# Kernel tuning notes

Hardware: AMD Instinct MI355X
Metric: run time of the kernel (lower is better)

The kernel has to match this reference:

```python
import jax, jax.numpy as jnp
import numpy as np

B, NW = 1024, 300
N = NW // 3          # 100 tokens (keypoints)
E = 5                # token dim after cat of PE(2): 3 + 2
H, D, L = 4, 64, 3   # heads, d_attention, layers


def setup_inputs() -> dict:
    key = jax.random.key(0)
    ks = jax.random.split(key, 8)
    s = jnp.float32(0.1)
    x = jax.random.normal(ks[0], (B, NW), dtype=jnp.float32)
    Wq = jax.random.normal(ks[1], (L, H, D, E), dtype=jnp.float32) * s  # per-head W_Q (no bias)
    Wk = jax.random.normal(ks[2], (L, H, D, E), dtype=jnp.float32) * s
    Wv = jax.random.normal(ks[3], (L, H, D, E), dtype=jnp.float32) * s
    Wo = jax.random.normal(ks[4], (L, E, H * D), dtype=jnp.float32) * s  # MHA output proj (no bias)
    Wf = jax.random.normal(ks[5], (L, E, E), dtype=jnp.float32) * s      # FFN linear
    bf = jax.random.normal(ks[6], (L, E), dtype=jnp.float32) * s
    g1 = jnp.ones((L, E), dtype=jnp.float32)
    b1 = jnp.zeros((L, E), dtype=jnp.float32)
    g2 = jnp.ones((L, E), dtype=jnp.float32)
    b2 = jnp.zeros((L, E), dtype=jnp.float32)
    return dict(x=x, Wq=Wq, Wk=Wk, Wv=Wv, Wo=Wo, Wf=Wf, bf=bf,
                g1=g1, b1=b1, g2=g2, b2=b2)


def _layer_norm(x, g, b, eps=1e-5):
    mu = jnp.mean(x, axis=-1, keepdims=True)
    var = jnp.mean((x - mu) ** 2, axis=-1, keepdims=True)  # biased, like torch LN
    return (x - mu) / jnp.sqrt(var + eps) * g + b


def reference(x, Wq, Wk, Wv, Wo, Wf, bf, g1, b1, g2, b2):
    kp = x.reshape(B, N, 3)                      # 'b (n d) -> b n d', d=3
    mask = kp[:, :, -1] > 0                      # [B,N] keypoint confidence mask
    # PositionalEncoding(d_model=2, kind='cat'): div_term=[1] -> pe=[sin(pos),cos(pos)]
    pos = jnp.arange(N, dtype=jnp.float32)
    pe = jnp.stack([jnp.sin(pos), jnp.cos(pos)], axis=-1)         # [N,2]
    out = jnp.concatenate([kp, jnp.broadcast_to(pe, (B, N, 2))], axis=-1)  # [B,N,5]
    out = jnp.where(mask[:, :, None], out, jnp.float32(0.0))      # out[~mask]=0

    pair = mask[:, None, None, :] & mask[:, None, :, None]        # [B,1,N,N]
    neg = -jnp.finfo(jnp.float32).max
    scale = jnp.float32(1.0 / np.sqrt(D))
    for l in range(L):
        # per-head projections (heads vectorized over h)
        q = jnp.einsum('bne,hde->bhnd', out, Wq[l])
        k = jnp.einsum('bne,hde->bhnd', out, Wk[l])
        v = jnp.einsum('bne,hde->bhnd', out, Wv[l])
        dots = jnp.einsum('bhid,bhjd->bhij', q, k) * scale        # [B,H,N,N]
        dots = jnp.where(pair, dots, neg)
        attn = jax.nn.softmax(dots, axis=-1)
        o = jnp.einsum('bhij,bhjd->bhid', attn, v)                # [B,H,N,D]
        o = o.transpose(0, 2, 1, 3).reshape(B, N, H * D)          # concat heads
        attn_out = o @ Wo[l].T                                    # [B,N,E]
        ln1 = _layer_norm(attn_out + out, g1[l], b1[l])
        ffn = jax.nn.relu(ln1 @ Wf[l].T + bf[l])
        out = _layer_norm(ffn + ln1, g2[l], b2[l])
    return out
```

## Files before the change

### kernel.cpp

```cpp
#include <hip/hip_runtime.h>
#include <math.h>

#define NTOK 100
#define EDIM 5
#define NH   4
#define NL   3
#define DD   64
#define BLK  256

__global__ void precompute_mp(const float* __restrict__ Wq,
                              const float* __restrict__ Wk,
                              const float* __restrict__ Wv,
                              const float* __restrict__ Wo,
                              float* __restrict__ mp) {
  int r = blockIdx.x * blockDim.x + threadIdx.x;
  if (r >= 600) return;
  int which = r / 300;
  int q = r % 300;
  int l = q / 100, rem = q % 100;
  int h = rem / 25, ef = rem % 25;
  int e = ef / 5, f = ef % 5;
  float acc = 0.f;
  if (which == 0) {
    const float* wq = Wq + ((l*NH + h)*DD)*EDIM;
    const float* wk = Wk + ((l*NH + h)*DD)*EDIM;
    #pragma unroll 8
    for (int d = 0; d < DD; ++d) acc += wq[d*EDIM + e] * wk[d*EDIM + f];
    acc *= 0.125f;
  } else {
    const float* wv = Wv + ((l*NH + h)*DD)*EDIM;
    const float* wo = Wo + (l*EDIM + f)*(NH*DD) + h*DD;
    #pragma unroll 8
    for (int d = 0; d < DD; ++d) acc += wv[d*EDIM + e] * wo[d];
  }
  mp[which*960 + ((l*NH + h)*EDIM + e)*8 + f] = acc;
}

__global__ __launch_bounds__(BLK) void encoder_kernel(
    const float* __restrict__ x,
    const float* __restrict__ mp,
    const float* __restrict__ Wf,
    const float* __restrict__ bfv,
    const float* __restrict__ g1,
    const float* __restrict__ b1,
    const float* __restrict__ g2,
    const float* __restrict__ b2,
    float* __restrict__ out)
{
  const int b = blockIdx.x, t = threadIdx.x;

  __shared__ float4 s_MP4[480];
  __shared__ float4 s_o4[NTOK+2];
  __shared__ float  s_o1[NTOK+2];
  __shared__ float4 s_u4[NH][NTOK+2];
  __shared__ float  s_u1[NH][NTOK+2];
  __shared__ float  s_c [NH][NTOK+1][EDIM];
  __shared__ float  s_cs[NH][EDIM];
  __shared__ int    s_cidx[NTOK];
  __shared__ unsigned long long s_bal[2];

  const float* mpf = (const float*)s_MP4;

  for (int r = t; r < 480; r += BLK) s_MP4[r] = ((const float4*)mp)[r];

  float k0=0.f, k1=0.f, k2=0.f, msk=0.f;
  if (t < NTOK) {
    k0 = x[b*300 + 3*t];
    k1 = x[b*300 + 3*t + 1];
    k2 = x[b*300 + 3*t + 2];
    msk = (k2 > 0.f) ? 1.f : 0.f;
  }
  unsigned long long bal = __ballot(t < NTOK && msk != 0.f);
  if (t == 0)  s_bal[0] = bal;
  if (t == 64) s_bal[1] = bal;
  __syncthreads();
  const unsigned long long bw0 = s_bal[0], bw1 = s_bal[1];
  const int nm = __popcll(bw0) + __popcll(bw1);
  if (t < NTOK) {
    int lane = t & 63;
    unsigned long long lm = (lane == 0) ? 0ull : ((1ull << lane) - 1ull);
    int pre = (t < 64) ? __popcll(bw0 & lm) : (__popcll(bw0) + __popcll(bw1 & lm));
    if (msk != 0.f) {
      s_o4[pre] = make_float4(k0, k1, k2, sinf((float)t));
      s_o1[pre] = cosf((float)t);
      s_cidx[t] = pre;
    } else {
      s_cidx[t] = nm;
    }
  }
  if (t == 0) {
    s_o4[nm]   = make_float4(0.f,0.f,0.f,0.f); s_o1[nm]   = 0.f;
    s_o4[nm+1] = make_float4(0.f,0.f,0.f,0.f); s_o1[nm+1] = 0.f;
  }
  __syncthreads();

  const int hp   = (nm + 2) >> 1;
  const int natt = 4 * hp;
  const bool task = (t < natt);
  int h = 0, i0 = 0, i1 = 0, i1r = 0;
  if (task) {
    h = t / hp; i0 = t - h*hp; i1 = i0 + hp;
    i1r = (i1 <= nm) ? i1 : nm;
  }
  const bool iscs = (!task) && (t - natt < 20);
  int csh = 0, cse = 0;
  if (iscs) { int idx = t - natt; csh = idx / 5; cse = idx - csh*5; }

  for (int l = 0; l < NL; ++l) {
    float a0[5], a1[5];
    if (task) {
      const float* Mh = mpf + ((l*NH + h)*EDIM)*8;
      const float* Ph = Mh + 960;
      float4 oA = s_o4[i0];  float oA4 = s_o1[i0];
      float4 oB = s_o4[i1r]; float oB4 = s_o1[i1r];
      float oa[5] = {oA.x, oA.y, oA.z, oA.w, oA4};
      float ob[5] = {oB.x, oB.y, oB.z, oB.w, oB4};
      float u0[5], u1v[5];
      #pragma unroll
      for (int f = 0; f < 5; ++f) { a0[f]=0.f; a1[f]=0.f; u0[f]=0.f; u1v[f]=0.f; }
      #pragma unroll
      for (int e = 0; e < 5; ++e) {
        float4 mr = *(const float4*)(Mh + e*8); float m4 = Mh[e*8+4];
        float4 pr = *(const float4*)(Ph + e*8); float p4 = Ph[e*8+4];
        float va = oa[e], vb = ob[e];
        a0[0] += va*mr.x; a0[1] += va*mr.y; a0[2] += va*mr.z; a0[3] += va*mr.w; a0[4] += va*m4;
        a1[0] += vb*mr.x; a1[1] += vb*mr.y; a1[2] += vb*mr.z; a1[3] += vb*mr.w; a1[4] += vb*m4;
        u0[0] += va*pr.x; u0[1] += va*pr.y; u0[2] += va*pr.z; u0[3] += va*pr.w; u0[4] += va*p4;
        u1v[0]+= vb*pr.x; u1v[1]+= vb*pr.y; u1v[2]+= vb*pr.z; u1v[3]+= vb*pr.w; u1v[4]+= vb*p4;
      }
      s_u4[h][i0]  = make_float4(u0[0], u0[1], u0[2], u0[3]);  s_u1[h][i0]  = u0[4];
      s_u4[h][i1r] = make_float4(u1v[0],u1v[1],u1v[2],u1v[3]); s_u1[h][i1r] = u1v[4];
    }
    __syncthreads();

    if (task) {
      const float4* __restrict__ pu4 = &s_u4[h][0];
      const float*  __restrict__ pu1 = &s_u1[h][0];
      float ls0 = 0.f, ls1 = 0.f;
      float c00=0.f,c01=0.f,c02=0.f,c03=0.f,c04=0.f;
      float c10=0.f,c11=0.f,c12=0.f,c13=0.f,c14=0.f;
      #pragma unroll 4
      for (int j = 0; j < nm; ++j) {
        float4 oj = s_o4[j]; float oe = s_o1[j];
        float4 uj = pu4[j];  float ue = pu1[j];
        float s0 = a0[0]*oj.x + a0[1]*oj.y + a0[2]*oj.z + a0[3]*oj.w + a0[4]*oe;
        float s1 = a1[0]*oj.x + a1[1]*oj.y + a1[2]*oj.z + a1[3]*oj.w + a1[4]*oe;
        float p0 = __expf(s0), p1 = __expf(s1);
        ls0 += p0; ls1 += p1;
        c00 += p0*uj.x; c01 += p0*uj.y; c02 += p0*uj.z; c03 += p0*uj.w; c04 += p0*ue;
        c10 += p1*uj.x; c11 += p1*uj.y; c12 += p1*uj.z; c13 += p1*uj.w; c14 += p1*ue;
      }
      if (i0 < nm) {
        float r0 = 1.f / ls0;
        s_c[h][i0][0]=c00*r0; s_c[h][i0][1]=c01*r0; s_c[h][i0][2]=c02*r0;
        s_c[h][i0][3]=c03*r0; s_c[h][i0][4]=c04*r0;
      }
      if (i1 < nm) {
        float r1 = 1.f / ls1;
        s_c[h][i1][0]=c10*r1; s_c[h][i1][1]=c11*r1; s_c[h][i1][2]=c12*r1;
        s_c[h][i1][3]=c13*r1; s_c[h][i1][4]=c14*r1;
      }
    } else if (iscs) {
      float acc = 0.f;
      if (cse < 4) { for (int j = 0; j < nm; ++j) acc += ((const float*)&s_u4[csh][j])[cse]; }
      else         { for (int j = 0; j < nm; ++j) acc += s_u1[csh][j]; }
      s_cs[csh][cse] = acc;
    }
    __syncthreads();

    if (t <= nm) {
      int i = t;
      float4 ov = s_o4[i]; float ov4 = s_o1[i];
      float o[5] = {ov.x, ov.y, ov.z, ov.w, ov4};
      float y[5];
      if (i < nm) {
        #pragma unroll
        for (int e = 0; e < 5; ++e)
          y[e] = o[e] + s_c[0][i][e] + s_c[1][i][e] + s_c[2][i][e] + s_c[3][i][e];
      } else {
        float w = (float)(NTOK - nm);
        #pragma unroll
        for (int e = 0; e < 5; ++e) {
          float sum = 0.f;
          #pragma unroll
          for (int hh = 0; hh < NH; ++hh) {
            float ur = (e < 4) ? ((const float*)&s_u4[hh][nm])[e] : s_u1[hh][nm];
            sum += s_cs[hh][e] + w*ur;
          }
          y[e] = o[e] + sum * 0.01f;
        }
      }
      float mu = 0.2f*(y[0]+y[1]+y[2]+y[3]+y[4]);
      float var = 0.f;
      #pragma unroll
      for (int e = 0; e < 5; ++e) { float d = y[e]-mu; var += d*d; }
      var *= 0.2f;
      float inv = 1.f / sqrtf(var + 1e-5f);
      float ln1[5];
      #pragma unroll
      for (int e = 0; e < 5; ++e) ln1[e] = (y[e]-mu)*inv*g1[l*5+e] + b1[l*5+e];
      float r2[5];
      #pragma unroll
      for (int e = 0; e < 5; ++e) {
        float acc = bfv[l*5+e];
        #pragma unroll
        for (int f = 0; f < 5; ++f) acc += ln1[f]*Wf[(l*5+e)*5+f];
        acc = acc > 0.f ? acc : 0.f;
        r2[e] = acc + ln1[e];
      }
      float mu2 = 0.2f*(r2[0]+r2[1]+r2[2]+r2[3]+r2[4]);
      float var2 = 0.f;
      #pragma unroll
      for (int e = 0; e < 5; ++e) { float d = r2[e]-mu2; var2 += d*d; }
      var2 *= 0.2f;
      float inv2 = 1.f / sqrtf(var2 + 1e-5f);
      #pragma unroll
      for (int e = 0; e < 5; ++e) {
        float no = (r2[e]-mu2)*inv2*g2[l*5+e] + b2[l*5+e];
        if (e == 0) { float4 tmp = s_o4[i]; tmp.x = no; s_o4[i] = tmp; }
      }
      float no0 = (r2[0]-mu2)*inv2*g2[l*5+0] + b2[l*5+0];
      float no1 = (r2[1]-mu2)*inv2*g2[l*5+1] + b2[l*5+1];
      float no2 = (r2[2]-mu2)*inv2*g2[l*5+2] + b2[l*5+2];
      float no3 = (r2[3]-mu2)*inv2*g2[l*5+3] + b2[l*5+3];
      float no4 = (r2[4]-mu2)*inv2*g2[l*5+4] + b2[l*5+4];
      s_o4[i] = make_float4(no0, no1, no2, no3);
      s_o1[i] = no4;
    }
    __syncthreads();
  }

  for (int r = t; r < NTOK*EDIM; r += BLK) {
    int i = r / EDIM;
    int e = r - i*EDIM;
    int c = s_cidx[i];
    float v = (e < 4) ? ((const float*)&s_o4[c])[e] : s_o1[c];
    out[b*(NTOK*EDIM) + r] = v;
  }
}

extern "C" void kernel_launch(void* const* d_in, const int* in_sizes, int n_in,
                              void* d_out, int out_size, void* d_ws, size_t ws_size,
                              hipStream_t stream) {
  const float* x  = (const float*)d_in[0];
  const float* Wq = (const float*)d_in[1];
  const float* Wk = (const float*)d_in[2];
  const float* Wv = (const float*)d_in[3];
  const float* Wo = (const float*)d_in[4];
  const float* Wf = (const float*)d_in[5];
  const float* bf = (const float*)d_in[6];
  const float* g1 = (const float*)d_in[7];
  const float* b1 = (const float*)d_in[8];
  const float* g2 = (const float*)d_in[9];
  const float* b2 = (const float*)d_in[10];
  float* outp = (float*)d_out;
  float* mp   = (float*)d_ws;

  precompute_mp<<<3, BLK, 0, stream>>>(Wq, Wk, Wv, Wo, mp);
  encoder_kernel<<<1024, BLK, 0, stream>>>(x, mp, Wf, bf, g1, b1, g2, b2, outp);
}
```

Before: 121.4 us.

## Aggregate attention-weighted tokens before value projection and split key range

The attention loop now accumulates softmax-weighted raw token vectors and applies the fused V·O projection once per query, instead of projecting every key first. This removes the per-layer U computation phase, one barrier and the column-sum helper threads. Keys are split across two thread groups when enough threads are free, and partial sums are combined in the residual stage. The weight precompute is also restructured to use per-(layer,head) blocks that stage weights in shared memory.

```diff
diff --git a/kernel.cpp b/kernel.cpp
--- a/kernel.cpp
+++ b/kernel.cpp
@@ -13,27 +13,40 @@
                               const float* __restrict__ Wv,
                               const float* __restrict__ Wo,
                               float* __restrict__ mp) {
-  int r = blockIdx.x * blockDim.x + threadIdx.x;
-  if (r >= 600) return;
-  int which = r / 300;
-  int q = r % 300;
-  int l = q / 100, rem = q % 100;
-  int h = rem / 25, ef = rem % 25;
-  int e = ef / 5, f = ef % 5;
-  float acc = 0.f;
+  const int blk = blockIdx.x;
+  const int which = blk / 12;
+  const int rem = blk % 12;
+  const int l = rem / 4, h = rem % 4;
+  const int t = threadIdx.x;
+
+  __shared__ float A[320];
+  __shared__ float Bsh[320];
+
+  const float* wa = (which ? Wv : Wq) + (l*NH + h)*DD*EDIM;
+  for (int r = t; r < 320; r += 64) A[r] = wa[r];
   if (which == 0) {
-    const float* wq = Wq + ((l*NH + h)*DD)*EDIM;
-    const float* wk = Wk + ((l*NH + h)*DD)*EDIM;
-    #pragma unroll 8
-    for (int d = 0; d < DD; ++d) acc += wq[d*EDIM + e] * wk[d*EDIM + f];
-    acc *= 0.125f;
+    const float* wk = Wk + (l*NH + h)*DD*EDIM;
+    for (int r = t; r < 320; r += 64) Bsh[r] = wk[r];
   } else {
-    const float* wv = Wv + ((l*NH + h)*DD)*EDIM;
-    const float* wo = Wo + (l*EDIM + f)*(NH*DD) + h*DD;
-    #pragma unroll 8
-    for (int d = 0; d < DD; ++d) acc += wv[d*EDIM + e] * wo[d];
-  }
-  mp[which*960 + ((l*NH + h)*EDIM + e)*8 + f] = acc;
+    for (int r = t; r < 320; r += 64) {
+      int f = r >> 6, d = r & 63;
+      Bsh[r] = Wo[(l*EDIM + f)*(NH*DD) + h*DD + d];
+    }
+  }
+  __syncthreads();
+  if (t < 25) {
+    int e = t / 5, f = t % 5;
+    float acc = 0.f;
+    if (which == 0) {
+      #pragma unroll 8
+      for (int d = 0; d < DD; ++d) acc += A[d*5+e] * Bsh[d*5+f];
+      acc *= 0.125f;
+    } else {
+      #pragma unroll 8
+      for (int d = 0; d < DD; ++d) acc += A[d*5+e] * Bsh[f*64+d];
+    }
+    mp[which*960 + ((l*NH + h)*EDIM + e)*8 + f] = acc;
+  }
 }
 
 __global__ __launch_bounds__(BLK) void encoder_kernel(
@@ -52,10 +65,8 @@
   __shared__ float4 s_MP4[480];
   __shared__ float4 s_o4[NTOK+2];
   __shared__ float  s_o1[NTOK+2];
-  __shared__ float4 s_u4[NH][NTOK+2];
-  __shared__ float  s_u1[NH][NTOK+2];
-  __shared__ float  s_c [NH][NTOK+1][EDIM];
-  __shared__ float  s_cs[NH][EDIM];
+  __shared__ float4 s_w4[2][NH][NTOK+2];
+  __shared__ float2 s_w2[2][NH][NTOK+2];
   __shared__ int    s_cidx[NTOK];
   __shared__ unsigned long long s_bal[2];
 
@@ -95,101 +106,96 @@
   __syncthreads();
 
   const int hp   = (nm + 2) >> 1;
-  const int natt = 4 * hp;
-  const bool task = (t < natt);
-  int h = 0, i0 = 0, i1 = 0, i1r = 0;
+  const int natt = NH * hp;
+  const int nsplit = (2*natt <= BLK) ? 2 : 1;
+  const bool task = (t < natt*nsplit);
+  int h = 0, i0 = 0, i1 = 0, i1r = 0, jlo = 0, jhi = 0;
+  bool rep0 = false, rep1 = false, w1ok = false;
   if (task) {
-    h = t / hp; i0 = t - h*hp; i1 = i0 + hp;
+    int g  = t / natt;
+    int tt = t - g*natt;
+    h = tt / hp; i0 = tt - h*hp; i1 = i0 + hp;
     i1r = (i1 <= nm) ? i1 : nm;
-  }
-  const bool iscs = (!task) && (t - natt < 20);
-  int csh = 0, cse = 0;
-  if (iscs) { int idx = t - natt; csh = idx / 5; cse = idx - csh*5; }
+    w1ok = (i1 <= nm);
+    rep0 = (i0 == nm); rep1 = (i1 == nm);
+    int jmid = nm >> 1;
+    if (nsplit == 2) { jlo = g ? jmid : 0; jhi = g ? nm : jmid; }
+    else             { jlo = 0; jhi = nm; }
+  }
+  const int wg = task ? (t / natt) : 0;
 
   for (int l = 0; l < NL; ++l) {
-    float a0[5], a1[5];
     if (task) {
       const float* Mh = mpf + ((l*NH + h)*EDIM)*8;
-      const float* Ph = Mh + 960;
       float4 oA = s_o4[i0];  float oA4 = s_o1[i0];
       float4 oB = s_o4[i1r]; float oB4 = s_o1[i1r];
       float oa[5] = {oA.x, oA.y, oA.z, oA.w, oA4};
       float ob[5] = {oB.x, oB.y, oB.z, oB.w, oB4};
-      float u0[5], u1v[5];
-      #pragma unroll
-      for (int f = 0; f < 5; ++f) { a0[f]=0.f; a1[f]=0.f; u0[f]=0.f; u1v[f]=0.f; }
+      float a0[5], a1[5];
+      #pragma unroll
+      for (int f = 0; f < 5; ++f) { a0[f] = 0.f; a1[f] = 0.f; }
       #pragma unroll
       for (int e = 0; e < 5; ++e) {
         float4 mr = *(const float4*)(Mh + e*8); float m4 = Mh[e*8+4];
-        float4 pr = *(const float4*)(Ph + e*8); float p4 = Ph[e*8+4];
         float va = oa[e], vb = ob[e];
         a0[0] += va*mr.x; a0[1] += va*mr.y; a0[2] += va*mr.z; a0[3] += va*mr.w; a0[4] += va*m4;
         a1[0] += vb*mr.x; a1[1] += vb*mr.y; a1[2] += vb*mr.z; a1[3] += vb*mr.w; a1[4] += vb*m4;
-        u0[0] += va*pr.x; u0[1] += va*pr.y; u0[2] += va*pr.z; u0[3] += va*pr.w; u0[4] += va*p4;
-        u1v[0]+= vb*pr.x; u1v[1]+= vb*pr.y; u1v[2]+= vb*pr.z; u1v[3]+= vb*pr.w; u1v[4]+= vb*p4;
-      }
-      s_u4[h][i0]  = make_float4(u0[0], u0[1], u0[2], u0[3]);  s_u1[h][i0]  = u0[4];
-      s_u4[h][i1r] = make_float4(u1v[0],u1v[1],u1v[2],u1v[3]); s_u1[h][i1r] = u1v[4];
-    }
-    __syncthreads();
-
-    if (task) {
-      const float4* __restrict__ pu4 = &s_u4[h][0];
-      const float*  __restrict__ pu1 = &s_u1[h][0];
-      float ls0 = 0.f, ls1 = 0.f;
-      float c00=0.f,c01=0.f,c02=0.f,c03=0.f,c04=0.f;
-      float c10=0.f,c11=0.f,c12=0.f,c13=0.f,c14=0.f;
+      }
+
+      float ls0=0.f, ls1=0.f;
+      float w00=0.f,w01=0.f,w02=0.f,w03=0.f,w04=0.f;
+      float w10=0.f,w11=0.f,w12=0.f,w13=0.f,w14=0.f;
       #pragma unroll 4
-      for (int j = 0; j < nm; ++j) {
+      for (int j = jlo; j < jhi; ++j) {
         float4 oj = s_o4[j]; float oe = s_o1[j];
-        float4 uj = pu4[j];  float ue = pu1[j];
         float s0 = a0[0]*oj.x + a0[1]*oj.y + a0[2]*oj.z + a0[3]*oj.w + a0[4]*oe;
         float s1 = a1[0]*oj.x + a1[1]*oj.y + a1[2]*oj.z + a1[3]*oj.w + a1[4]*oe;
-        float p0 = __expf(s0), p1 = __expf(s1);
+        float p0 = rep0 ? 1.f : __expf(s0);
+        float p1 = rep1 ? 1.f : __expf(s1);
         ls0 += p0; ls1 += p1;
-        c00 += p0*uj.x; c01 += p0*uj.y; c02 += p0*uj.z; c03 += p0*uj.w; c04 += p0*ue;
-        c10 += p1*uj.x; c11 += p1*uj.y; c12 += p1*uj.z; c13 += p1*uj.w; c14 += p1*ue;
-      }
-      if (i0 < nm) {
-        float r0 = 1.f / ls0;
-        s_c[h][i0][0]=c00*r0; s_c[h][i0][1]=c01*r0; s_c[h][i0][2]=c02*r0;
-        s_c[h][i0][3]=c03*r0; s_c[h][i0][4]=c04*r0;
-      }
-      if (i1 < nm) {
-        float r1 = 1.f / ls1;
-        s_c[h][i1][0]=c10*r1; s_c[h][i1][1]=c11*r1; s_c[h][i1][2]=c12*r1;
-        s_c[h][i1][3]=c13*r1; s_c[h][i1][4]=c14*r1;
-      }
-    } else if (iscs) {
-      float acc = 0.f;
-      if (cse < 4) { for (int j = 0; j < nm; ++j) acc += ((const float*)&s_u4[csh][j])[cse]; }
-      else         { for (int j = 0; j < nm; ++j) acc += s_u1[csh][j]; }
-      s_cs[csh][cse] = acc;
+        w00 += p0*oj.x; w01 += p0*oj.y; w02 += p0*oj.z; w03 += p0*oj.w; w04 += p0*oe;
+        w10 += p1*oj.x; w11 += p1*oj.y; w12 += p1*oj.z; w13 += p1*oj.w; w14 += p1*oe;
+      }
+      s_w4[wg][h][i0] = make_float4(w00, w01, w02, w03);
+      s_w2[wg][h][i0] = make_float2(w04, ls0);
+      if (w1ok) {
+        s_w4[wg][h][i1] = make_float4(w10, w11, w12, w13);
+        s_w2[wg][h][i1] = make_float2(w14, ls1);
+      }
     }
     __syncthreads();
 
     if (t <= nm) {
       int i = t;
+      bool rep = (i == nm);
       float4 ov = s_o4[i]; float ov4 = s_o1[i];
       float o[5] = {ov.x, ov.y, ov.z, ov.w, ov4};
-      float y[5];
-      if (i < nm) {
+      float wext = rep ? (float)(NTOK - nm) : 0.f;
+      float c[5] = {0.f, 0.f, 0.f, 0.f, 0.f};
+      #pragma unroll
+      for (int hh = 0; hh < NH; ++hh) {
+        float4 wa = s_w4[0][hh][i]; float2 wb = s_w2[0][hh][i];
+        float w[5] = {wa.x, wa.y, wa.z, wa.w, wb.x};
+        float ls = wb.y;
+        if (nsplit == 2) {
+          float4 wa2 = s_w4[1][hh][i]; float2 wb2 = s_w2[1][hh][i];
+          w[0] += wa2.x; w[1] += wa2.y; w[2] += wa2.z; w[3] += wa2.w; w[4] += wb2.x;
+          ls += wb2.y;
+        }
         #pragma unroll
-        for (int e = 0; e < 5; ++e)
-          y[e] = o[e] + s_c[0][i][e] + s_c[1][i][e] + s_c[2][i][e] + s_c[3][i][e];
-      } else {
-        float w = (float)(NTOK - nm);
+        for (int e = 0; e < 5; ++e) w[e] += wext * o[e];
+        float inv = 1.f / (rep ? (float)NTOK : ls);
+        const float* Ph = mpf + 960 + ((l*NH + hh)*EDIM)*8;
         #pragma unroll
         for (int e = 0; e < 5; ++e) {
-          float sum = 0.f;
-          #pragma unroll
-          for (int hh = 0; hh < NH; ++hh) {
-            float ur = (e < 4) ? ((const float*)&s_u4[hh][nm])[e] : s_u1[hh][nm];
-            sum += s_cs[hh][e] + w*ur;
-          }
-          y[e] = o[e] + sum * 0.01f;
+          float4 pr = *(const float4*)(Ph + e*8); float p4 = Ph[e*8+4];
+          float we = w[e] * inv;
+          c[0] += we*pr.x; c[1] += we*pr.y; c[2] += we*pr.z; c[3] += we*pr.w; c[4] += we*p4;
         }
       }
+      float y[5];
+      #pragma unroll
+      for (int e = 0; e < 5; ++e) y[e] = o[e] + c[e];
       float mu = 0.2f*(y[0]+y[1]+y[2]+y[3]+y[4]);
       float var = 0.f;
       #pragma unroll
@@ -214,11 +220,6 @@
       for (int e = 0; e < 5; ++e) { float d = r2[e]-mu2; var2 += d*d; }
       var2 *= 0.2f;
       float inv2 = 1.f / sqrtf(var2 + 1e-5f);
-      #pragma unroll
-      for (int e = 0; e < 5; ++e) {
-        float no = (r2[e]-mu2)*inv2*g2[l*5+e] + b2[l*5+e];
-        if (e == 0) { float4 tmp = s_o4[i]; tmp.x = no; s_o4[i] = tmp; }
-      }
       float no0 = (r2[0]-mu2)*inv2*g2[l*5+0] + b2[l*5+0];
       float no1 = (r2[1]-mu2)*inv2*g2[l*5+1] + b2[l*5+1];
       float no2 = (r2[2]-mu2)*inv2*g2[l*5+2] + b2[l*5+2];
@@ -256,6 +257,6 @@
   float* outp = (float*)d_out;
   float* mp   = (float*)d_ws;
 
-  precompute_mp<<<3, BLK, 0, stream>>>(Wq, Wk, Wv, Wo, mp);
+  precompute_mp<<<24, 64, 0, stream>>>(Wq, Wk, Wv, Wo, mp);
   encoder_kernel<<<1024, BLK, 0, stream>>>(x, mp, Wf, bf, g1, b1, g2, b2, outp);
 }
```

Measured after the change: 119.2 us. About the same (-1.8%).
